# Kernel tuning notes

Measured on AMD Instinct MI355X. Metric: run time of the kernel, lower is better.

The kernel has to match this reference:

```python
import jax, jax.numpy as jnp
import numpy as np
import math

B, S, HID, NH = 2, 2048, 1024, 16
HD = HID // NH


def setup_inputs() -> dict:
    key = jax.random.key(0)
    ks = jax.random.split(key, 6)
    scale = 0.02
    return {
        "hidden_states": jax.random.normal(ks[0], (B, S, HID), dtype=jnp.float32),
        "attention_mask": jnp.ones((B, S), dtype=jnp.float32),
        "Wq": jax.random.normal(ks[1], (HID, HID), dtype=jnp.float32) * scale,
        "bq": jnp.zeros((HID,), dtype=jnp.float32),
        "Wk": jax.random.normal(ks[2], (HID, HID), dtype=jnp.float32) * scale,
        "bk": jnp.zeros((HID,), dtype=jnp.float32),
        "Wv": jax.random.normal(ks[3], (HID, HID), dtype=jnp.float32) * scale,
        "bv": jnp.zeros((HID,), dtype=jnp.float32),
        "Wo": jax.random.normal(ks[4], (HID, HID), dtype=jnp.float32) * scale,
        "bo": jnp.zeros((HID,), dtype=jnp.float32),
        "beta": jnp.zeros((1,), dtype=jnp.float32),
        "gamma": jnp.ones((1,), dtype=jnp.float32),
    }


def reference(hidden_states, attention_mask, Wq, bq, Wk, bk, Wv, bv, Wo, bo, beta, gamma):
    b, s, h = hidden_states.shape

    def proj(W, bias):
        # torch Linear: x @ W.T + b ; then split heads -> [B, NH, S, HD]
        y = jnp.einsum('bsh,oh->bso', hidden_states, W) + bias
        return y.reshape(b, s, NH, HD).transpose(0, 2, 1, 3)

    q = proj(Wq, bq)
    k = proj(Wk, bk)
    v = proj(Wv, bv)

    scores = jnp.einsum('bnsd,bntd->bnst', q, k) / math.sqrt(HD)  # [B,NH,S,S]
    # extended mask: [B,1,1,S]; additive -1e4 on masked positions
    scores = scores + (1.0 - attention_mask)[:, None, None, :] * (-10000.0)

    # ConsMax: exp(scores - beta - rowmax) / gamma (no sum normalization)
    shifted = scores - beta
    shifted = shifted - jnp.max(shifted, axis=-1, keepdims=True)
    probs = jnp.exp(shifted) / gamma  # dropout p=0 -> identity

    ctx = jnp.einsum('bnst,bntd->bnsd', probs, v)  # [B,NH,S,HD]
    ctx = ctx.transpose(0, 2, 1, 3).reshape(b, s, h)
    return jnp.einsum('bsh,oh->bso', ctx, Wo) + bo
```

## Files before the change

kernel.cpp:

```cpp
#include <hip/hip_runtime.h>
#include <hip/hip_bf16.h>


typedef unsigned short u16;
typedef __attribute__((ext_vector_type(8))) short short8;
typedef __attribute__((ext_vector_type(4))) float floatx4;

constexpr int B_  = 2;
constexpr int S_  = 2048;
constexpr int HID = 1024;
constexpr int NH  = 16;
constexpr int HD  = 64;
constexpr int M_  = B_ * S_;

constexpr float LOG2E   = 1.4426950408889634f;
constexpr float QSCALE  = 0.125f * LOG2E;
constexpr float MSCALE  = -10000.0f * LOG2E;

__device__ __forceinline__ float us2f(u16 u) {
    union { unsigned int i; float f; } x;
    x.i = ((unsigned int)u) << 16;
    return x.f;
}
__device__ __forceinline__ u16 f2us(float f) {
    union { float f; unsigned int i; } x;
    x.f = f;
    unsigned int r = x.i + 0x7FFFu + ((x.i >> 16) & 1u);
    return (u16)(r >> 16);
}
__device__ __forceinline__ unsigned pk2(float a, float b) {
    __hip_bfloat162 h = __float22bfloat162_rn(make_float2(a, b));
    unsigned u; __builtin_memcpy(&u, &h, 4); return u;
}
__device__ __forceinline__ void async_lds16(const u16* g, u16* l) {
    __builtin_amdgcn_global_load_lds(
        (const __attribute__((address_space(1))) unsigned int*)g,
        (__attribute__((address_space(3))) unsigned int*)l, 16, 0, 0);
}

__global__ __launch_bounds__(256)
void cvt_all(const float* __restrict__ hs, const float* __restrict__ Wq,
             const float* __restrict__ Wk, const float* __restrict__ Wv,
             const float* __restrict__ Wo,
             u16* __restrict__ hs_bf, u16* __restrict__ Wcat,
             u16* __restrict__ Wo_bf)
{
    const int bid = blockIdx.x;
    const float* src;
    u16* dst;
    size_t base;
    if (bid < 4096) {
        src = hs; dst = hs_bf; base = (size_t)bid * 1024;
    } else if (bid < 7168) {
        const int s = (bid - 4096) >> 10;
        src = (s == 0) ? Wq : (s == 1) ? Wk : Wv;
        dst = Wcat + (size_t)s * 1048576;
        base = (size_t)((bid - 4096) & 1023) * 1024;
    } else {
        src = Wo; dst = Wo_bf; base = (size_t)(bid - 7168) * 1024;
    }
    const size_t i = base + threadIdx.x * 4;
    float4 t = *(const float4*)(src + i);
    uint2 o = { pk2(t.x, t.y), pk2(t.z, t.w) };
    *(uint2*)(dst + i) = o;
}

__global__ __launch_bounds__(256)
void qkv_gemm(const u16* __restrict__ hs_bf, const u16* __restrict__ Wcat,
              const float* __restrict__ bq, const float* __restrict__ bk,
              const float* __restrict__ bv,
              u16* __restrict__ Qo, u16* __restrict__ Ko, u16* __restrict__ VT)
{
    __shared__ u16 Alds[8192];
    __shared__ u16 Blds[8192];

    const int tid = threadIdx.x;
    const int id  = blockIdx.x;
    const int xcd = id & 7, jb = id >> 3;
    const int m0  = (xcd * 4 + (jb & 3)) * 128;
    const int n0g = (jb >> 2) * 128;
    const int p   = n0g >> 10;
    const int n0  = n0g & 1023;
    const u16*   Wb = Wcat + (size_t)p * 1048576;
    const float* bi = (p == 0) ? bq : (p == 1) ? bk : bv;
    const float  osc = (p == 0) ? QSCALE : 1.0f;

    const int w = tid >> 6, l = tid & 63;
    const int quad = l >> 4, l16 = l & 15;
    const int wy = w >> 1, wx = w & 1;

    floatx4 acc[4][4];
    #pragma unroll
    for (int i = 0; i < 4; ++i)
        #pragma unroll
        for (int j = 0; j < 4; ++j) acc[i][j] = (floatx4){0.f, 0.f, 0.f, 0.f};

    for (int k0 = 0; k0 < HID; k0 += 64) {
        __syncthreads();
        #pragma unroll
        for (int c = 0; c < 2; ++c) {
            const int s = w * 2 + c;
            #pragma unroll
            for (int t = 0; t < 2; ++t) {
                async_lds16(hs_bf + (size_t)(m0 + s * 16 + l16) * HID + k0 + t * 32 + quad * 8,
                            &Alds[s * 1024 + t * 512]);
                async_lds16(Wb + (size_t)(n0 + s * 16 + l16) * HID + k0 + t * 32 + quad * 8,
                            &Blds[s * 1024 + t * 512]);
            }
        }
        __syncthreads();

        #pragma unroll
        for (int t = 0; t < 2; ++t) {
            short8 afr[4], bfr[4];
            #pragma unroll
            for (int i = 0; i < 4; ++i)
                afr[i] = *(const short8*)&Alds[(wy*4 + i) * 1024 + t * 512 + l * 8];
            #pragma unroll
            for (int j = 0; j < 4; ++j)
                bfr[j] = *(const short8*)&Blds[(wx*4 + j) * 1024 + t * 512 + l * 8];
            #pragma unroll
            for (int i = 0; i < 4; ++i)
                #pragma unroll
                for (int j = 0; j < 4; ++j)
                    acc[i][j] = __builtin_amdgcn_mfma_f32_16x16x32_bf16(afr[i], bfr[j], acc[i][j], 0, 0, 0);
        }
    }

    #pragma unroll
    for (int i = 0; i < 4; ++i)
        #pragma unroll
        for (int j = 0; j < 4; ++j) {
            const int nn   = n0 + wx * 64 + j * 16 + l16;
            const int head = nn >> 6, dd = nn & 63;
            const float bb_ = bi[nn];
            const int mmb = m0 + wy * 64 + i * 16 + quad * 4;
            const int b = mmb >> 11, ss = mmb & (S_ - 1);
            if (p == 2) {
                uint2 st = { pk2(acc[i][j][0] + bb_, acc[i][j][1] + bb_),
                             pk2(acc[i][j][2] + bb_, acc[i][j][3] + bb_) };
                *(uint2*)(VT + (((size_t)(b * NH + head)) * HD + dd) * S_ + ss) = st;
            } else {
                u16* Out = (p == 0) ? Qo : Ko;
                #pragma unroll
                for (int rg = 0; rg < 4; ++rg)
                    Out[(((size_t)b * NH + head) * S_ + ss + rg) * HD + dd] =
                        f2us((acc[i][j][rg] + bb_) * osc);
            }
        }
}

__global__ __launch_bounds__(256)
void attn6(const u16* __restrict__ Qg, const u16* __restrict__ Kg,
           const u16* __restrict__ VTg, const float* __restrict__ mask,
           const float* __restrict__ gamma, u16* __restrict__ ctx)
{
    __shared__ u16 Kb[8192];
    __shared__ u16 Vb[8192];
    __shared__ float maskb[128];

    const int tid = threadIdx.x;
    const int w = tid >> 6, l = tid & 63;
    const int quad = l >> 4, l16 = l & 15;
    const int id  = blockIdx.x;
    const int xcd = id & 7, jb = id >> 3;
    const int bh  = xcd * 4 + (jb >> 5);
    const int qb  = jb & 31;
    const int b0  = bh >> 4, h = bh & (NH - 1);

    const u16* Qb  = Qg  + (size_t)bh * S_ * HD;
    const u16* Kbg = Kg  + (size_t)bh * S_ * HD;
    const u16* Vbg = VTg + (size_t)bh * HD * S_;

    short8 qf[2];
    #pragma unroll
    for (int t = 0; t < 2; ++t)
        qf[t] = *(const short8*)(Qb + ((size_t)qb * 64 + 16 * w + l16) * HD + 32 * t + quad * 8);

    floatx4 o_acc[4];
    #pragma unroll
    for (int jn = 0; jn < 4; ++jn) o_acc[jn] = (floatx4){0.f, 0.f, 0.f, 0.f};
    float m_run = -1e30f;

    u16* Pal = Kb + w * 2048;

    for (int kt = 0; kt < S_ / 128; ++kt) {
        float mnext = 0.0f;
        if (tid < 128)
            mnext = (1.0f - mask[(size_t)b0 * S_ + kt * 128 + tid]) * MSCALE;
        __syncthreads();
        #pragma unroll
        for (int c = 0; c < 2; ++c) {
            const int s = w * 2 + c;
            #pragma unroll
            for (int t = 0; t < 2; ++t)
                async_lds16(Kbg + ((size_t)kt * 128 + s * 16 + l16) * HD + t * 32 + quad * 8,
                            &Kb[s * 1024 + t * 512]);
        }
        #pragma unroll
        for (int tt = 0; tt < 4; ++tt)
            async_lds16(Vbg + (size_t)(w * 16 + l16) * S_ + kt * 128 + tt * 32 + quad * 8,
                        &Vb[w * 2048 + tt * 512]);
        if (tid < 128) maskb[tid] = mnext;
        __syncthreads();

        floatx4 st4[8];
        #pragma unroll
        for (int j = 0; j < 8; ++j) st4[j] = (floatx4){0.f, 0.f, 0.f, 0.f};
        #pragma unroll
        for (int t = 0; t < 2; ++t)
            #pragma unroll
            for (int j = 0; j < 8; ++j) {
                short8 kf = *(const short8*)&Kb[j * 1024 + t * 512 + l * 8];
                st4[j] = __builtin_amdgcn_mfma_f32_16x16x32_bf16(kf, qf[t], st4[j], 0, 0, 0);
            }

        uint2 pr[8];
        #pragma unroll
        for (int j = 0; j < 8; ++j) {
            #pragma unroll
            for (int i = 0; i < 4; ++i) {
                st4[j][i] += maskb[j * 16 + quad * 4 + i];
                m_run = fmaxf(m_run, st4[j][i]);
            }
            pr[j].x = pk2(exp2f(st4[j][0]), exp2f(st4[j][1]));
            pr[j].y = pk2(exp2f(st4[j][2]), exp2f(st4[j][3]));
        }
        __syncthreads();

        #pragma unroll
        for (int j = 0; j < 8; ++j) {
            const int off = (j >> 1) * 512
                          + (l16 + 16 * ((j & 1) * 2 + (quad >> 1))) * 8
                          + (quad & 1) * 4;
            *(uint2*)&Pal[off] = pr[j];
        }

        #pragma unroll
        for (int tt = 0; tt < 4; ++tt) {
            short8 pf = *(const short8*)&Pal[tt * 512 + l * 8];
            #pragma unroll
            for (int jn = 0; jn < 4; ++jn) {
                short8 vf = *(const short8*)&Vb[jn * 2048 + tt * 512 + l * 8];
                o_acc[jn] = __builtin_amdgcn_mfma_f32_16x16x32_bf16(pf, vf, o_acc[jn], 0, 0, 0);
            }
        }
    }

    float mx = m_run;
    mx = fmaxf(mx, __shfl_xor(mx, 16, 64));
    mx = fmaxf(mx, __shfl_xor(mx, 32, 64));
    const float ig = 1.0f / gamma[0];
    #pragma unroll
    for (int i = 0; i < 4; ++i) {
        const float si = exp2f(-__shfl(mx, quad * 4 + i, 64)) * ig;
        const int srow = qb * 64 + 16 * w + quad * 4 + i;
        #pragma unroll
        for (int jn = 0; jn < 4; ++jn)
            ctx[((size_t)(b0 * S_ + srow)) * HID + h * HD + jn * 16 + l16] =
                f2us(o_acc[jn][i] * si);
    }
}

__global__ __launch_bounds__(256)
void out_gemm(const u16* __restrict__ ctx, const u16* __restrict__ Wo_bf,
              const float* __restrict__ bo, float* __restrict__ out)
{
    __shared__ u16 Alds[8192];
    __shared__ u16 Blds[4096];

    const int tid = threadIdx.x;
    const int id  = blockIdx.x;
    const int xcd = id & 7, jb = id >> 3;
    const int m0  = (xcd * 4 + (jb & 3)) * 128;
    const int n0  = (jb >> 2) * 64;

    const int w = tid >> 6, l = tid & 63;
    const int quad = l >> 4, l16 = l & 15;

    floatx4 acc[2][4];
    #pragma unroll
    for (int i = 0; i < 2; ++i)
        #pragma unroll
        for (int j = 0; j < 4; ++j) acc[i][j] = (floatx4){0.f, 0.f, 0.f, 0.f};

    for (int k0 = 0; k0 < HID; k0 += 64) {
        __syncthreads();
        #pragma unroll
        for (int c = 0; c < 2; ++c) {
            const int s = w * 2 + c;
            #pragma unroll
            for (int t = 0; t < 2; ++t)
                async_lds16(ctx + (size_t)(m0 + s * 16 + l16) * HID + k0 + t * 32 + quad * 8,
                            &Alds[s * 1024 + t * 512]);
        }
        #pragma unroll
        for (int t = 0; t < 2; ++t)
            async_lds16(Wo_bf + (size_t)(n0 + w * 16 + l16) * HID + k0 + t * 32 + quad * 8,
                        &Blds[w * 1024 + t * 512]);
        __syncthreads();

        #pragma unroll
        for (int t = 0; t < 2; ++t) {
            short8 afr[2], bfr[4];
            #pragma unroll
            for (int i = 0; i < 2; ++i)
                afr[i] = *(const short8*)&Alds[(w*2 + i) * 1024 + t * 512 + l * 8];
            #pragma unroll
            for (int j = 0; j < 4; ++j)
                bfr[j] = *(const short8*)&Blds[j * 1024 + t * 512 + l * 8];
            #pragma unroll
            for (int i = 0; i < 2; ++i)
                #pragma unroll
                for (int j = 0; j < 4; ++j)
                    acc[i][j] = __builtin_amdgcn_mfma_f32_16x16x32_bf16(afr[i], bfr[j], acc[i][j], 0, 0, 0);
        }
    }

    #pragma unroll
    for (int i = 0; i < 2; ++i)
        #pragma unroll
        for (int j = 0; j < 4; ++j) {
            const int nn = n0 + j * 16 + l16;
            const float bb_ = bo[nn];
            #pragma unroll
            for (int rg = 0; rg < 4; ++rg) {
                const int mm = m0 + w * 32 + i * 16 + quad * 4 + rg;
                out[(size_t)mm * HID + nn] = acc[i][j][rg] + bb_;
            }
        }
}

extern "C" void kernel_launch(void* const* d_in, const int* in_sizes, int n_in,
                              void* d_out, int out_size, void* d_ws, size_t ws_size,
                              hipStream_t stream)
{
    const float* hs    = (const float*)d_in[0];
    const float* mask  = (const float*)d_in[1];
    const float* Wq    = (const float*)d_in[2];
    const float* bq    = (const float*)d_in[3];
    const float* Wk    = (const float*)d_in[4];
    const float* bk    = (const float*)d_in[5];
    const float* Wv    = (const float*)d_in[6];
    const float* bv    = (const float*)d_in[7];
    const float* Wo    = (const float*)d_in[8];
    const float* bo    = (const float*)d_in[9];
    const float* gamma = (const float*)d_in[11];
    float* out = (float*)d_out;

    const size_t tsz = (size_t)B_ * NH * S_ * HD;
    u16* q     = (u16*)d_ws;
    u16* vT    = q + tsz;
    u16* Wcat  = vT + tsz;
    u16* Wo_bf = Wcat + 3u * 1048576u;
    u16* ctx   = Wo_bf + 1048576u;
    u16* hs_bf = (u16*)d_out;
    u16* kbuf  = hs_bf + tsz;

    cvt_all<<<dim3(8192), 256, 0, stream>>>(hs, Wq, Wk, Wv, Wo, hs_bf, Wcat, Wo_bf);
    qkv_gemm<<<dim3(768), 256, 0, stream>>>(hs_bf, Wcat, bq, bk, bv, q, kbuf, vT);
    attn6<<<dim3(1024), 256, 0, stream>>>(q, kbuf, vT, mask, gamma, ctx);
    out_gemm<<<dim3(512), 256, 0, stream>>>(ctx, Wo_bf, bo, out);
}
```

Measured before the change: 263.5 us.

## Double query rows per attention block to reuse K/V tiles, drop mask LDS staging

The attention kernel now handles 128 query rows per block (32 per wave, two 16-row sub-tiles) rather than 64, so each K and V tile loaded into LDS feeds twice as many MFMAs and the grid halves. P gets a dedicated LDS buffer instead of aliasing the K buffer, which removes one barrier per iteration. Mask values are read straight from global memory as float4, dropping the shared mask buffer. The cost is more registers and LDS per block (launch bounds set to 2 blocks per CU) and half as many blocks to spread across CUs.

```diff
diff --git a/kernel.cpp b/kernel.cpp
--- a/kernel.cpp
+++ b/kernel.cpp
@@ -17,11 +17,6 @@
 constexpr float QSCALE  = 0.125f * LOG2E;
 constexpr float MSCALE  = -10000.0f * LOG2E;
 
-__device__ __forceinline__ float us2f(u16 u) {
-    union { unsigned int i; float f; } x;
-    x.i = ((unsigned int)u) << 16;
-    return x.f;
-}
 __device__ __forceinline__ u16 f2us(float f) {
     union { float f; unsigned int i; } x;
     x.f = f;
@@ -150,44 +145,46 @@
         }
 }
 
-__global__ __launch_bounds__(256)
-void attn6(const u16* __restrict__ Qg, const u16* __restrict__ Kg,
+__global__ __launch_bounds__(256, 2)
+void attn7(const u16* __restrict__ Qg, const u16* __restrict__ Kg,
            const u16* __restrict__ VTg, const float* __restrict__ mask,
            const float* __restrict__ gamma, u16* __restrict__ ctx)
 {
     __shared__ u16 Kb[8192];
     __shared__ u16 Vb[8192];
-    __shared__ float maskb[128];
+    __shared__ u16 Pb[16384];
 
     const int tid = threadIdx.x;
     const int w = tid >> 6, l = tid & 63;
     const int quad = l >> 4, l16 = l & 15;
     const int id  = blockIdx.x;
     const int xcd = id & 7, jb = id >> 3;
-    const int bh  = xcd * 4 + (jb >> 5);
-    const int qb  = jb & 31;
+    const int bh  = xcd * 4 + (jb >> 4);
+    const int qb  = jb & 15;
     const int b0  = bh >> 4, h = bh & (NH - 1);
 
-    const u16* Qb  = Qg  + (size_t)bh * S_ * HD;
-    const u16* Kbg = Kg  + (size_t)bh * S_ * HD;
-    const u16* Vbg = VTg + (size_t)bh * HD * S_;
-
-    short8 qf[2];
-    #pragma unroll
-    for (int t = 0; t < 2; ++t)
-        qf[t] = *(const short8*)(Qb + ((size_t)qb * 64 + 16 * w + l16) * HD + 32 * t + quad * 8);
-
-    floatx4 o_acc[4];
-    #pragma unroll
-    for (int jn = 0; jn < 4; ++jn) o_acc[jn] = (floatx4){0.f, 0.f, 0.f, 0.f};
-    float m_run = -1e30f;
-
-    u16* Pal = Kb + w * 2048;
+    const u16* Qb    = Qg  + (size_t)bh * S_ * HD;
+    const u16* Kbg   = Kg  + (size_t)bh * S_ * HD;
+    const u16* Vbg   = VTg + (size_t)bh * HD * S_;
+    const float* mG  = mask + (size_t)b0 * S_;
+
+    short8 qf[2][2];
+    #pragma unroll
+    for (int u = 0; u < 2; ++u)
+        #pragma unroll
+        for (int t = 0; t < 2; ++t)
+            qf[u][t] = *(const short8*)(Qb + ((size_t)qb * 128 + 32 * w + u * 16 + l16) * HD + 32 * t + quad * 8);
+
+    floatx4 o_acc[2][4];
+    #pragma unroll
+    for (int u = 0; u < 2; ++u)
+        #pragma unroll
+        for (int jn = 0; jn < 4; ++jn) o_acc[u][jn] = (floatx4){0.f, 0.f, 0.f, 0.f};
+    float m_run[2] = { -1e30f, -1e30f };
+
+    u16* Pw = Pb + w * 4096;
 
     for (int kt = 0; kt < S_ / 128; ++kt) {
-        float mnext = 0.0f;
-        if (tid < 128)
-            mnext = (1.0f - mask[(size_t)b0 * S_ + kt * 128 + tid]) * MSCALE;
         __syncthreads();
         #pragma unroll
         for (int c = 0; c < 2; ++c) {
@@ -201,64 +198,69 @@
         for (int tt = 0; tt < 4; ++tt)
             async_lds16(Vbg + (size_t)(w * 16 + l16) * S_ + kt * 128 + tt * 32 + quad * 8,
                         &Vb[w * 2048 + tt * 512]);
-        if (tid < 128) maskb[tid] = mnext;
-        __syncthreads();
-
-        floatx4 st4[8];
-        #pragma unroll
-        for (int j = 0; j < 8; ++j) st4[j] = (floatx4){0.f, 0.f, 0.f, 0.f};
-        #pragma unroll
-        for (int t = 0; t < 2; ++t)
-            #pragma unroll
-            for (int j = 0; j < 8; ++j) {
-                short8 kf = *(const short8*)&Kb[j * 1024 + t * 512 + l * 8];
-                st4[j] = __builtin_amdgcn_mfma_f32_16x16x32_bf16(kf, qf[t], st4[j], 0, 0, 0);
-            }
-
-        uint2 pr[8];
+        __syncthreads();
+
+        float4 mv[8];
         #pragma unroll
         for (int j = 0; j < 8; ++j) {
-            #pragma unroll
-            for (int i = 0; i < 4; ++i) {
-                st4[j][i] += maskb[j * 16 + quad * 4 + i];
-                m_run = fmaxf(m_run, st4[j][i]);
-            }
-            pr[j].x = pk2(exp2f(st4[j][0]), exp2f(st4[j][1]));
-            pr[j].y = pk2(exp2f(st4[j][2]), exp2f(st4[j][3]));
-        }
-        __syncthreads();
+            float4 r = *(const float4*)(mG + kt * 128 + j * 16 + quad * 4);
+            mv[j].x = (1.0f - r.x) * MSCALE;
+            mv[j].y = (1.0f - r.y) * MSCALE;
+            mv[j].z = (1.0f - r.z) * MSCALE;
+            mv[j].w = (1.0f - r.w) * MSCALE;
+        }
 
         #pragma unroll
         for (int j = 0; j < 8; ++j) {
+            short8 kf0 = *(const short8*)&Kb[j * 1024 + l * 8];
+            short8 kf1 = *(const short8*)&Kb[j * 1024 + 512 + l * 8];
+            floatx4 s0 = (floatx4){0.f, 0.f, 0.f, 0.f};
+            floatx4 s1 = (floatx4){0.f, 0.f, 0.f, 0.f};
+            s0 = __builtin_amdgcn_mfma_f32_16x16x32_bf16(kf0, qf[0][0], s0, 0, 0, 0);
+            s0 = __builtin_amdgcn_mfma_f32_16x16x32_bf16(kf1, qf[0][1], s0, 0, 0, 0);
+            s1 = __builtin_amdgcn_mfma_f32_16x16x32_bf16(kf0, qf[1][0], s1, 0, 0, 0);
+            s1 = __builtin_amdgcn_mfma_f32_16x16x32_bf16(kf1, qf[1][1], s1, 0, 0, 0);
+            s0[0] += mv[j].x; s0[1] += mv[j].y; s0[2] += mv[j].z; s0[3] += mv[j].w;
+            s1[0] += mv[j].x; s1[1] += mv[j].y; s1[2] += mv[j].z; s1[3] += mv[j].w;
+            m_run[0] = fmaxf(fmaxf(fmaxf(s0[0], s0[1]), fmaxf(s0[2], s0[3])), m_run[0]);
+            m_run[1] = fmaxf(fmaxf(fmaxf(s1[0], s1[1]), fmaxf(s1[2], s1[3])), m_run[1]);
+            uint2 p0 = { pk2(exp2f(s0[0]), exp2f(s0[1])), pk2(exp2f(s0[2]), exp2f(s0[3])) };
+            uint2 p1 = { pk2(exp2f(s1[0]), exp2f(s1[1])), pk2(exp2f(s1[2]), exp2f(s1[3])) };
             const int off = (j >> 1) * 512
                           + (l16 + 16 * ((j & 1) * 2 + (quad >> 1))) * 8
                           + (quad & 1) * 4;
-            *(uint2*)&Pal[off] = pr[j];
+            *(uint2*)&Pw[off]        = p0;
+            *(uint2*)&Pw[2048 + off] = p1;
         }
 
         #pragma unroll
         for (int tt = 0; tt < 4; ++tt) {
-            short8 pf = *(const short8*)&Pal[tt * 512 + l * 8];
+            short8 pf0 = *(const short8*)&Pw[tt * 512 + l * 8];
+            short8 pf1 = *(const short8*)&Pw[2048 + tt * 512 + l * 8];
             #pragma unroll
             for (int jn = 0; jn < 4; ++jn) {
                 short8 vf = *(const short8*)&Vb[jn * 2048 + tt * 512 + l * 8];
-                o_acc[jn] = __builtin_amdgcn_mfma_f32_16x16x32_bf16(pf, vf, o_acc[jn], 0, 0, 0);
+                o_acc[0][jn] = __builtin_amdgcn_mfma_f32_16x16x32_bf16(pf0, vf, o_acc[0][jn], 0, 0, 0);
+                o_acc[1][jn] = __builtin_amdgcn_mfma_f32_16x16x32_bf16(pf1, vf, o_acc[1][jn], 0, 0, 0);
             }
         }
     }
 
-    float mx = m_run;
-    mx = fmaxf(mx, __shfl_xor(mx, 16, 64));
-    mx = fmaxf(mx, __shfl_xor(mx, 32, 64));
     const float ig = 1.0f / gamma[0];
     #pragma unroll
-    for (int i = 0; i < 4; ++i) {
-        const float si = exp2f(-__shfl(mx, quad * 4 + i, 64)) * ig;
-        const int srow = qb * 64 + 16 * w + quad * 4 + i;
-        #pragma unroll
-        for (int jn = 0; jn < 4; ++jn)
-            ctx[((size_t)(b0 * S_ + srow)) * HID + h * HD + jn * 16 + l16] =
-                f2us(o_acc[jn][i] * si);
+    for (int u = 0; u < 2; ++u) {
+        float mx = m_run[u];
+        mx = fmaxf(mx, __shfl_xor(mx, 16, 64));
+        mx = fmaxf(mx, __shfl_xor(mx, 32, 64));
+        #pragma unroll
+        for (int i = 0; i < 4; ++i) {
+            const float si = exp2f(-__shfl(mx, quad * 4 + i, 64)) * ig;
+            const int srow = qb * 128 + 32 * w + u * 16 + quad * 4 + i;
+            #pragma unroll
+            for (int jn = 0; jn < 4; ++jn)
+                ctx[((size_t)(b0 * S_ + srow)) * HID + h * HD + jn * 16 + l16] =
+                    f2us(o_acc[u][jn][i] * si);
+        }
     }
 }
 
@@ -359,6 +361,6 @@
 
     cvt_all<<<dim3(8192), 256, 0, stream>>>(hs, Wq, Wk, Wv, Wo, hs_bf, Wcat, Wo_bf);
     qkv_gemm<<<dim3(768), 256, 0, stream>>>(hs_bf, Wcat, bq, bk, bv, q, kbuf, vT);
-    attn6<<<dim3(1024), 256, 0, stream>>>(q, kbuf, vT, mask, gamma, ctx);
+    attn7<<<dim3(512), 256, 0, stream>>>(q, kbuf, vT, mask, gamma, ctx);
     out_gemm<<<dim3(512), 256, 0, stream>>>(ctx, Wo_bf, bo, out);
 }
```

New measurement: 259.0 us. No clear change (-1.7%).
